# Optimization experiments

Hardware: AMD Instinct MI355X
Metric: run time of the kernel (lower is better)

Reference implementation:

```python
import jax, jax.numpy as jnp
import numpy as np

N, T = 32, 2048
ENC_DIM, DEC_DIM, ATT_DIM = 1024, 1024, 512
CONV_CH, LOC_CTX = 10, 64  # F conv kernel = 2*64+1 = 129 taps


def setup_inputs() -> dict:
    key = jax.random.key(0)
    ks = jax.random.split(key, 12)
    inv = lambda d: 1.0 / np.sqrt(d)
    return {
        "enc_pad": jax.random.normal(ks[0], (N, T, ENC_DIM), jnp.float32),
        "enc_len": jax.random.randint(ks[1], (N,), T // 2, T + 1),
        "dec_prev": jax.random.normal(ks[2], (N, DEC_DIM), jnp.float32),
        "ali_prev": jax.random.uniform(ks[3], (N, T), jnp.float32),
        # enc_proj: Linear(enc_dim, att_dim)
        "W_enc": jax.random.normal(ks[4], (ENC_DIM, ATT_DIM), jnp.float32) * inv(ENC_DIM),
        "b_enc": jax.random.normal(ks[5], (ATT_DIM,), jnp.float32) * 0.01,
        # dec_proj: Linear(dec_dim, att_dim, bias=False)
        "W_dec": jax.random.normal(ks[6], (DEC_DIM, ATT_DIM), jnp.float32) * inv(DEC_DIM),
        # F: Conv1d(1, conv_channels, 129, padding=64)  -> weight [C_out, C_in=1, K]
        "F_w": jax.random.normal(ks[7], (CONV_CH, 1, 2 * LOC_CTX + 1), jnp.float32) * inv(2 * LOC_CTX + 1),
        "F_b": jax.random.normal(ks[8], (CONV_CH,), jnp.float32) * 0.01,
        # att: Conv1d(conv_channels, att_dim, 1, bias=False) == pointwise mix [A, C]
        "W_att": jax.random.normal(ks[9], (ATT_DIM, CONV_CH), jnp.float32) * inv(CONV_CH),
        # w: Linear(att_dim, 1, bias=False)
        "w_vec": jax.random.normal(ks[10], (ATT_DIM,), jnp.float32) * inv(ATT_DIM),
    }


def reference(enc_pad, enc_len, dec_prev, ali_prev, W_enc, b_enc, W_dec, F_w, F_b, W_att, w_vec):
    n, t, _ = enc_pad.shape
    # enc_part: N x T x A (cached across decode steps in the original)
    enc_part = jnp.einsum("ntd,da->nta", enc_pad, W_enc) + b_enc
    # padding mask: True where t >= enc_len
    pad_mask = jnp.arange(t)[None, :] >= enc_len[:, None]  # N x T
    f_out = jax.lax.conv_general_dilated(
        ali_prev[:, None, :], F_w, window_strides=(1,),
        padding=[(LOC_CTX, LOC_CTX)],
        dimension_numbers=("NCH", "OIH", "NCH")) + F_b[None, :, None]
    # pointwise conv (att) then transpose(1,2): N x T x A
    att_part = jnp.einsum("nct,ac->nta", f_out, W_att)
    dec_part = dec_prev @ W_dec  # N x A
    sum_part = jnp.tanh(att_part + dec_part[:, None, :] + enc_part)  # N x T x A
    score = jnp.einsum("nta,a->nt", sum_part, w_vec)  # N x T
    score = jnp.where(pad_mask, -jnp.inf, score)
    ali = jax.nn.softmax(score, axis=-1)  # N x T
    ctx = jnp.einsum("nt,ntd->nd", ali, enc_pad)  # N x D_enc
    return ali, ctx
```

## Files before the change

### kernel.cpp

```cpp
#include <hip/hip_runtime.h>

typedef __attribute__((ext_vector_type(4))) float f32x4;
typedef __attribute__((ext_vector_type(8))) short s16x8;
typedef __attribute__((ext_vector_type(8))) unsigned short u16x8;
typedef __attribute__((address_space(1))) unsigned int g_uint;
typedef __attribute__((address_space(3))) unsigned int lds_uint;

#define T_LEN 2048
#define ENC_D 1024
#define ATT_D 512
#define CONV_C 10

static __device__ __forceinline__ unsigned short f2bf(float f) {
  unsigned int u = __float_as_uint(f);
  u += 0x7FFFu + ((u >> 16) & 1u);
  return (unsigned short)(u >> 16);
}

static __device__ __forceinline__ void gload16(const void* g, void* l) {
  __builtin_amdgcn_global_load_lds((const g_uint*)g, (lds_uint*)l, 16, 0, 0);
}

__global__ void k_wt(const float* __restrict__ W, unsigned short* __restrict__ Wt2) {
  __shared__ float tile[64][65];
  int k0 = blockIdx.x * 64, a0 = blockIdx.y * 64;
  int tid = threadIdx.x;
  int r = tid >> 2, cg = tid & 3;
  #pragma unroll
  for (int i = 0; i < 4; ++i) {
    f32x4 v = *reinterpret_cast<const f32x4*>(&W[(size_t)(k0 + r) * ATT_D + a0 + cg * 16 + i * 4]);
    tile[r][cg * 16 + i * 4 + 0] = v[0];
    tile[r][cg * 16 + i * 4 + 1] = v[1];
    tile[r][cg * 16 + i * 4 + 2] = v[2];
    tile[r][cg * 16 + i * 4 + 3] = v[3];
  }
  __syncthreads();
  int r2 = tid >> 2, kg = tid & 3;
  u16x8 o0, o1;
  #pragma unroll
  for (int j = 0; j < 8; ++j) o0[j] = f2bf(tile[kg * 16 + j][r2]);
  #pragma unroll
  for (int j = 0; j < 8; ++j) o1[j] = f2bf(tile[kg * 16 + 8 + j][r2]);
  int a = a0 + r2;
  int kt = blockIdx.x;
  int q0 = kg * 2, q1 = q0 + 1;
  size_t tb = (size_t)kt * 32768 + (a >> 3) * 512;
  int s7 = a & 7;
  *reinterpret_cast<u16x8*>(&Wt2[tb + q0 * 64 + (s7 ^ q0) * 8]) = o0;
  *reinterpret_cast<u16x8*>(&Wt2[tb + q1 * 64 + (s7 ^ q1) * 8]) = o1;
}

__global__ void k_watt(const float* __restrict__ Wa, unsigned short* __restrict__ Wt2) {
  int a = blockIdx.x * 256 + threadIdx.x;
  size_t tb = (size_t)16 * 32768 + (a >> 3) * 512;
  int s7 = a & 7;
  #pragma unroll
  for (int j = 0; j < 8; ++j) {
    u16x8 v;
    #pragma unroll
    for (int e = 0; e < 8; ++e) {
      int c = j * 8 + e;
      v[e] = (c < CONV_C) ? f2bf(Wa[a * CONV_C + c]) : (unsigned short)0;
    }
    *reinterpret_cast<u16x8*>(&Wt2[tb + j * 64 + (s7 ^ j) * 8]) = v;
  }
}

__global__ void k_conv(const float* __restrict__ ali, const float* __restrict__ Fw,
                       const float* __restrict__ Fb, float* __restrict__ fout) {
  int b = blockIdx.x;
  int tb = b & 7, nc = b >> 3;
  int c = nc % CONV_C, n = nc / CONV_C;
  __shared__ float sa[384];
  __shared__ float sw[129];
  int tid = threadIdx.x;
  int t0 = tb * 256;
  for (int i = tid; i < 384; i += 256) {
    int t = t0 - 64 + i;
    sa[i] = (t >= 0 && t < T_LEN) ? ali[n * T_LEN + t] : 0.f;
  }
  if (tid < 129) sw[tid] = Fw[c * 129 + tid];
  __syncthreads();
  float acc = Fb[c];
  #pragma unroll 8
  for (int k = 0; k < 129; ++k) acc += sw[k] * sa[tid + k];
  fout[(size_t)(n * CONV_C + c) * T_LEN + t0 + tid] = acc;
}

__global__ void k_dec(const float* __restrict__ dec_prev, const float* __restrict__ Wd,
                      const float* __restrict__ benc, float* __restrict__ dec_ws) {
  __shared__ float red[256];
  int b = blockIdx.x;
  int n = b >> 4, ac = b & 15;
  int tid = threadIdx.x;
  int dg = tid >> 5, al = tid & 31;
  int a = ac * 32 + al;
  const float* dp = dec_prev + (size_t)n * 1024 + dg * 128;
  const float* wp = Wd + (size_t)(dg * 128) * ATT_D + a;
  float s = 0.f;
  #pragma unroll 4
  for (int i = 0; i < 128; ++i) s += dp[i] * wp[(size_t)i * ATT_D];
  red[tid] = s;
  __syncthreads();
  if (dg == 0) {
    float t = benc[a];
    #pragma unroll
    for (int g = 0; g < 8; ++g) t += red[g * 32 + al];
    dec_ws[(size_t)n * ATT_D + a] = t;
  }
}

__global__ __launch_bounds__(512, 2) void k_score(
    const float* __restrict__ enc, const unsigned short* __restrict__ Wt2,
    const float* __restrict__ fout, const float* __restrict__ dec_ws,
    const float* __restrict__ w_vec, const int* __restrict__ enc_len,
    float* __restrict__ score_ws) {
  __shared__ __align__(16) char smem[163840];

  int bid = blockIdx.x;
  int half = bid >> 8, p = bid & 255;
  int n = p >> 3, i0 = p & 7;
  int tt = half ? (15 - i0) : i0;
  int t0b = tt * 128;
  if (t0b >= enc_len[n]) return;

  int tid = threadIdx.x;
  int w = tid >> 6, lane = tid & 63;
  int l15 = lane & 15, q = lane >> 4;
  int wm = w >> 2, wn = w & 3;

  const float* Ab = enc + ((size_t)n * T_LEN + t0b) * ENC_D;
  int arow = tid >> 2, aq4 = tid & 3;
  const float* Asrc = Ab + (size_t)arow * ENC_D + aq4 * 16;
  int c0 = aq4 * 2, c1 = c0 + 1;
  int awoff0 = 65536 + (arow >> 3) * 1024 + c0 * 128 + ((arow & 7) ^ c0) * 16;
  int awoff1 = 65536 + (arow >> 3) * 1024 + c1 * 128 + ((arow & 7) ^ c1) * 16;

  int x0 = (l15 & 7) ^ q;
  int ck0 = q * 128 + x0 * 16;
  int ck1 = 512 + q * 128 + (x0 ^ 4) * 16;
  int rgA = wm * 8 + (l15 >> 3);
  int rgB = wn * 16 + (l15 >> 3);

  char* b0 = smem;
  char* b1 = smem + 81920;

  f32x4 acc[4][8];
  #pragma unroll
  for (int m = 0; m < 4; ++m)
    #pragma unroll
    for (int nf = 0; nf < 8; ++nf)
      acc[m][nf] = (f32x4){0.f, 0.f, 0.f, 0.f};

  f32x4 xA0, xA1, xA2, xA3;

  auto STAGE = [&](int kt, char* buf) {
    const float* pA = Asrc + (size_t)kt * 64;
    xA0 = *reinterpret_cast<const f32x4*>(pA);
    xA1 = *reinterpret_cast<const f32x4*>(pA + 4);
    xA2 = *reinterpret_cast<const f32x4*>(pA + 8);
    xA3 = *reinterpret_cast<const f32x4*>(pA + 12);
    const unsigned short* s = Wt2 + (size_t)kt * 32768 + tid * 8;
    #pragma unroll
    for (int i = 0; i < 8; ++i)
      gload16(s + i * 4096, buf + tid * 16 + i * 8192);
  };
  auto WRITEA = [&](char* buf) {
    union { u16x8 v; unsigned int u[4]; } p0, p1;
    asm("v_cvt_pk_bf16_f32 %0, %1, %2" : "=v"(p0.u[0]) : "v"(xA0[0]), "v"(xA0[1]));
    asm("v_cvt_pk_bf16_f32 %0, %1, %2" : "=v"(p0.u[1]) : "v"(xA0[2]), "v"(xA0[3]));
    asm("v_cvt_pk_bf16_f32 %0, %1, %2" : "=v"(p0.u[2]) : "v"(xA1[0]), "v"(xA1[1]));
    asm("v_cvt_pk_bf16_f32 %0, %1, %2" : "=v"(p0.u[3]) : "v"(xA1[2]), "v"(xA1[3]));
    asm("v_cvt_pk_bf16_f32 %0, %1, %2" : "=v"(p1.u[0]) : "v"(xA2[0]), "v"(xA2[1]));
    asm("v_cvt_pk_bf16_f32 %0, %1, %2" : "=v"(p1.u[1]) : "v"(xA2[2]), "v"(xA2[3]));
    asm("v_cvt_pk_bf16_f32 %0, %1, %2" : "=v"(p1.u[2]) : "v"(xA3[0]), "v"(xA3[1]));
    asm("v_cvt_pk_bf16_f32 %0, %1, %2" : "=v"(p1.u[3]) : "v"(xA3[2]), "v"(xA3[3]));
    *reinterpret_cast<u16x8*>(buf + awoff0) = p0.v;
    *reinterpret_cast<u16x8*>(buf + awoff1) = p1.v;
  };
  auto compute = [&](const char* buf) {
    s16x8 af0[4], af1[4];
    #pragma unroll
    for (int m = 0; m < 4; ++m) {
      af0[m] = *reinterpret_cast<const s16x8*>(buf + 65536 + (rgA + m * 2) * 1024 + ck0);
      af1[m] = *reinterpret_cast<const s16x8*>(buf + 65536 + (rgA + m * 2) * 1024 + ck1);
    }
    __builtin_amdgcn_s_setprio(1);
    #pragma unroll
    for (int nf = 0; nf < 8; ++nf) {
      s16x8 bf0 = *reinterpret_cast<const s16x8*>(buf + (rgB + nf * 2) * 1024 + ck0);
      s16x8 bf1 = *reinterpret_cast<const s16x8*>(buf + (rgB + nf * 2) * 1024 + ck1);
      #pragma unroll
      for (int m = 0; m < 4; ++m) {
        acc[m][nf] = __builtin_amdgcn_mfma_f32_16x16x32_bf16(af0[m], bf0, acc[m][nf], 0, 0, 0);
        acc[m][nf] = __builtin_amdgcn_mfma_f32_16x16x32_bf16(af1[m], bf1, acc[m][nf], 0, 0, 0);
      }
    }
    __builtin_amdgcn_s_setprio(0);
  };

  if (tid < 128) {
    float fv[CONV_C];
    #pragma unroll
    for (int c = 0; c < CONV_C; ++c)
      fv[c] = fout[((size_t)n * CONV_C + c) * T_LEN + t0b + tid];
    char* base = b0 + 65536 + (tid >> 3) * 1024;
    int s7 = tid & 7;
    #pragma unroll
    for (int j = 0; j < 8; ++j) {
      u16x8 v;
      #pragma unroll
      for (int e = 0; e < 8; ++e) {
        int c = j * 8 + e;
        v[e] = (c < CONV_C) ? f2bf(fv[c]) : (unsigned short)0;
      }
      *reinterpret_cast<u16x8*>(base + j * 128 + (s7 ^ j) * 16) = v;
    }
  }
  {
    const unsigned short* s = Wt2 + (size_t)16 * 32768 + tid * 8;
    #pragma unroll
    for (int i = 0; i < 8; ++i)
      gload16(s + i * 4096, b0 + tid * 16 + i * 8192);
  }
  STAGE(0, b1);
  asm volatile("s_waitcnt vmcnt(0) lgkmcnt(0)" ::: "memory");
  __builtin_amdgcn_sched_barrier(0);
  __builtin_amdgcn_s_barrier();
  compute(b0);
  WRITEA(b1);

  char* pc = b1; char* pn = b0;
  for (int k = 0; k < 16; ++k) {
    asm volatile("s_waitcnt vmcnt(0) lgkmcnt(0)" ::: "memory");
    __builtin_amdgcn_sched_barrier(0);
    __builtin_amdgcn_s_barrier();
    if (k + 1 < 16) STAGE(k + 1, pn);
    compute(pc);
    if (k + 1 < 16) WRITEA(pn);
    char* t = pc; pc = pn; pn = t;
  }
  __syncthreads();

  float* d_lds = (float*)smem;
  float* w_lds = (float*)(smem + 2048);
  float* red   = (float*)(smem + 4096);
  d_lds[tid] = dec_ws[(size_t)n * ATT_D + tid];
  w_lds[tid] = w_vec[tid];
  __syncthreads();

  #pragma unroll
  for (int m = 0; m < 4; ++m) {
    #pragma unroll
    for (int j = 0; j < 4; ++j) {
      int ttl = wm * 64 + m * 16 + q * 4 + j;
      float s = 0.f;
      #pragma unroll
      for (int nf = 0; nf < 8; ++nf) {
        int cl = wn * 128 + nf * 16 + l15;
        float x = acc[m][nf][j] + d_lds[cl];
        float e = __expf(2.f * x);
        float th = 1.f - 2.f / (e + 1.f);
        s += w_lds[cl] * th;
      }
      float v = s;
      v += __shfl_xor(v, 1);
      v += __shfl_xor(v, 2);
      v += __shfl_xor(v, 4);
      v += __shfl_xor(v, 8);
      if (l15 == 0) red[wn * 128 + ttl] = v;
    }
  }
  __syncthreads();
  if (tid < 128) {
    float s = red[tid] + red[128 + tid] + red[256 + tid] + red[384 + tid];
    score_ws[(size_t)n * T_LEN + t0b + tid] = s;
  }
}

__global__ void k_softmax(const float* __restrict__ score_ws, const int* __restrict__ enc_len,
                          float* __restrict__ ali_out) {
  __shared__ float wmx[4], wsum[4];
  int n = blockIdx.x, tid = threadIdx.x;
  int len = enc_len[n];
  int w = tid >> 6, lane = tid & 63;
  float s[8], e[8];
  float mx = -1e30f;
  #pragma unroll
  for (int i = 0; i < 8; ++i) {
    int t = i * 256 + tid;
    float v = score_ws[n * T_LEN + t];
    s[i] = v;
    if (t < len) mx = fmaxf(mx, v);
  }
  #pragma unroll
  for (int off = 32; off; off >>= 1) mx = fmaxf(mx, __shfl_xor(mx, off));
  if (lane == 0) wmx[w] = mx;
  __syncthreads();
  mx = fmaxf(fmaxf(wmx[0], wmx[1]), fmaxf(wmx[2], wmx[3]));
  float sum = 0.f;
  #pragma unroll
  for (int i = 0; i < 8; ++i) {
    int t = i * 256 + tid;
    float v = (t < len) ? __expf(s[i] - mx) : 0.f;
    e[i] = v;
    sum += v;
  }
  #pragma unroll
  for (int off = 32; off; off >>= 1) sum += __shfl_xor(sum, off);
  if (lane == 0) wsum[w] = sum;
  __syncthreads();
  sum = wsum[0] + wsum[1] + wsum[2] + wsum[3];
  float inv = 1.f / sum;
  #pragma unroll
  for (int i = 0; i < 8; ++i) ali_out[n * T_LEN + i * 256 + tid] = e[i] * inv;
}

__global__ void k_ctx(const float* __restrict__ ali, const float* __restrict__ enc,
                      const int* __restrict__ enc_len, float* __restrict__ part) {
  int b = blockIdx.x;
  int n = b >> 5, tc = b & 31;
  int tid = threadIdx.x;
  if (tc * 64 >= enc_len[n]) {
    *reinterpret_cast<f32x4*>(&part[(size_t)b * ENC_D + tid * 4]) = (f32x4){0.f, 0.f, 0.f, 0.f};
    return;
  }
  f32x4 acc = (f32x4){0.f, 0.f, 0.f, 0.f};
  const float* ep = enc + (size_t)(n * T_LEN + tc * 64) * ENC_D + tid * 4;
  const float* ap = ali + n * T_LEN + tc * 64;
  #pragma unroll 4
  for (int i = 0; i < 64; ++i) {
    float a = ap[i];
    f32x4 ev = *reinterpret_cast<const f32x4*>(ep + (size_t)i * ENC_D);
    acc += ev * a;
  }
  *reinterpret_cast<f32x4*>(&part[(size_t)b * ENC_D + tid * 4]) = acc;
}

__global__ void k_ctx_red(const float* __restrict__ part, float* __restrict__ ctx_out) {
  int g = blockIdx.x * 256 + threadIdx.x;
  int n = g >> 10, d = g & 1023;
  float s = 0.f;
  #pragma unroll 8
  for (int tc = 0; tc < 32; ++tc) s += part[(size_t)(n * 32 + tc) * ENC_D + d];
  ctx_out[g] = s;
}

extern "C" void kernel_launch(void* const* d_in, const int* in_sizes, int n_in,
                              void* d_out, int out_size, void* d_ws, size_t ws_size,
                              hipStream_t stream) {
  const float* enc      = (const float*)d_in[0];
  const int*   enc_len  = (const int*)d_in[1];
  const float* dec_prev = (const float*)d_in[2];
  const float* ali_prev = (const float*)d_in[3];
  const float* W_enc    = (const float*)d_in[4];
  const float* b_enc    = (const float*)d_in[5];
  const float* W_dec    = (const float*)d_in[6];
  const float* F_w      = (const float*)d_in[7];
  const float* F_b      = (const float*)d_in[8];
  const float* W_att    = (const float*)d_in[9];
  const float* w_vec    = (const float*)d_in[10];
  float* out = (float*)d_out;

  char* ws = (char*)d_ws;
  unsigned short* Wt2 = (unsigned short*)ws;
  float* fout   = (float*)(ws + 1114112);
  float* dec_ws = (float*)(ws + 3735552);
  float* score  = (float*)(ws + 3801088);
  float* part   = (float*)(ws + 4063232);

  hipLaunchKernelGGL(k_wt, dim3(16, 8), dim3(256), 0, stream, W_enc, Wt2);
  hipLaunchKernelGGL(k_watt, dim3(2), dim3(256), 0, stream, W_att, Wt2);
  hipLaunchKernelGGL(k_conv, dim3(2560), dim3(256), 0, stream, ali_prev, F_w, F_b, fout);
  hipLaunchKernelGGL(k_dec, dim3(512), dim3(256), 0, stream, dec_prev, W_dec, b_enc, dec_ws);
  hipLaunchKernelGGL(k_score, dim3(512), dim3(512), 0, stream, enc, Wt2, fout, dec_ws, w_vec, enc_len, score);
  hipLaunchKernelGGL(k_softmax, dim3(32), dim3(256), 0, stream, score, enc_len, out);
  hipLaunchKernelGGL(k_ctx, dim3(1024), dim3(256), 0, stream, out, enc, enc_len, part);
  hipLaunchKernelGGL(k_ctx_red, dim3(128), dim3(256), 0, stream, part, out + 65536);
}
```

Measured before the change: 162.4 us.

## Shrink score GEMM tile to 64 rows and K-step 32 with 1024 blocks

The score kernel's block tile drops from 128 time rows with 8 waves to 64 rows with 4 waves, and its K step from 64 to 32. The launch grows to 1024 blocks and the LDS footprint shrinks, so more blocks fit per CU and the grid fills the GPU more evenly. The weight pre-pack layout changes to match the 32-wide K tiles. In exchange, W_enc is re-read twice as often per row of output, and the number of pipeline barriers doubles.

New measurement: 190.5 us. +17.3%, slower.

```diff
diff --git a/kernel.cpp b/kernel.cpp
--- a/kernel.cpp
+++ b/kernel.cpp
@@ -42,27 +42,28 @@
   #pragma unroll
   for (int j = 0; j < 8; ++j) o1[j] = f2bf(tile[kg * 16 + 8 + j][r2]);
   int a = a0 + r2;
-  int kt = blockIdx.x;
-  int q0 = kg * 2, q1 = q0 + 1;
-  size_t tb = (size_t)kt * 32768 + (a >> 3) * 512;
+  int k = k0 + kg * 16;
+  int kt = k >> 5;
+  int q0 = (k >> 3) & 3;
+  size_t tb = (size_t)kt * 16384 + (a >> 3) * 256;
   int s7 = a & 7;
   *reinterpret_cast<u16x8*>(&Wt2[tb + q0 * 64 + (s7 ^ q0) * 8]) = o0;
-  *reinterpret_cast<u16x8*>(&Wt2[tb + q1 * 64 + (s7 ^ q1) * 8]) = o1;
+  *reinterpret_cast<u16x8*>(&Wt2[tb + (q0 + 1) * 64 + (s7 ^ (q0 + 1)) * 8]) = o1;
 }
 
 __global__ void k_watt(const float* __restrict__ Wa, unsigned short* __restrict__ Wt2) {
   int a = blockIdx.x * 256 + threadIdx.x;
-  size_t tb = (size_t)16 * 32768 + (a >> 3) * 512;
+  size_t tb = (size_t)32 * 16384 + (a >> 3) * 256;
   int s7 = a & 7;
   #pragma unroll
-  for (int j = 0; j < 8; ++j) {
+  for (int q2 = 0; q2 < 4; ++q2) {
     u16x8 v;
     #pragma unroll
-    for (int e = 0; e < 8; ++e) {
-      int c = j * 8 + e;
-      v[e] = (c < CONV_C) ? f2bf(Wa[a * CONV_C + c]) : (unsigned short)0;
+    for (int j = 0; j < 8; ++j) {
+      int c = q2 * 8 + j;
+      v[j] = (c < CONV_C) ? f2bf(Wa[a * CONV_C + c]) : (unsigned short)0;
     }
-    *reinterpret_cast<u16x8*>(&Wt2[tb + j * 64 + (s7 ^ j) * 8]) = v;
+    *reinterpret_cast<u16x8*>(&Wt2[tb + q2 * 64 + (s7 ^ q2) * 8]) = v;
   }
 }
 
@@ -110,40 +111,35 @@
   }
 }
 
-__global__ __launch_bounds__(512, 2) void k_score(
+__global__ __launch_bounds__(256, 2) void k_score(
     const float* __restrict__ enc, const unsigned short* __restrict__ Wt2,
     const float* __restrict__ fout, const float* __restrict__ dec_ws,
     const float* __restrict__ w_vec, const int* __restrict__ enc_len,
     float* __restrict__ score_ws) {
-  __shared__ __align__(16) char smem[163840];
+  __shared__ __align__(16) char smem[73728];
 
   int bid = blockIdx.x;
-  int half = bid >> 8, p = bid & 255;
-  int n = p >> 3, i0 = p & 7;
-  int tt = half ? (15 - i0) : i0;
-  int t0b = tt * 128;
+  int n, tt;
+  if (bid < 512) { n = bid >> 4; tt = bid & 15; }
+  else { int p = bid - 512; n = p >> 4; tt = 16 + (p & 15); }
+  int t0b = tt * 64;
   if (t0b >= enc_len[n]) return;
 
   int tid = threadIdx.x;
-  int w = tid >> 6, lane = tid & 63;
+  int wn = tid >> 6, lane = tid & 63;
   int l15 = lane & 15, q = lane >> 4;
-  int wm = w >> 2, wn = w & 3;
 
   const float* Ab = enc + ((size_t)n * T_LEN + t0b) * ENC_D;
-  int arow = tid >> 2, aq4 = tid & 3;
-  const float* Asrc = Ab + (size_t)arow * ENC_D + aq4 * 16;
-  int c0 = aq4 * 2, c1 = c0 + 1;
-  int awoff0 = 65536 + (arow >> 3) * 1024 + c0 * 128 + ((arow & 7) ^ c0) * 16;
-  int awoff1 = 65536 + (arow >> 3) * 1024 + c1 * 128 + ((arow & 7) ^ c1) * 16;
-
-  int x0 = (l15 & 7) ^ q;
-  int ck0 = q * 128 + x0 * 16;
-  int ck1 = 512 + q * 128 + (x0 ^ 4) * 16;
-  int rgA = wm * 8 + (l15 >> 3);
-  int rgB = wn * 16 + (l15 >> 3);
+  int arow = tid >> 2, aq = tid & 3;
+  const float* Asrc = Ab + (size_t)arow * ENC_D + aq * 8;
+
+  int awoff = 32768 + (arow >> 3) * 512 + aq * 128 + ((arow & 7) ^ aq) * 16;
+  int swl = (l15 & 7) ^ q;
+  int aql = 32768 + (l15 >> 3) * 512 + q * 128 + swl * 16;
+  int bql = (wn * 16 + (l15 >> 3)) * 512 + q * 128 + swl * 16;
 
   char* b0 = smem;
-  char* b1 = smem + 81920;
+  char* b1 = smem + 36864;
 
   f32x4 acc[4][8];
   #pragma unroll
@@ -152,76 +148,64 @@
     for (int nf = 0; nf < 8; ++nf)
       acc[m][nf] = (f32x4){0.f, 0.f, 0.f, 0.f};
 
-  f32x4 xA0, xA1, xA2, xA3;
+  f32x4 xA0, xA1;
 
   auto STAGE = [&](int kt, char* buf) {
-    const float* pA = Asrc + (size_t)kt * 64;
+    const float* pA = Asrc + (size_t)kt * 32;
     xA0 = *reinterpret_cast<const f32x4*>(pA);
     xA1 = *reinterpret_cast<const f32x4*>(pA + 4);
-    xA2 = *reinterpret_cast<const f32x4*>(pA + 8);
-    xA3 = *reinterpret_cast<const f32x4*>(pA + 12);
-    const unsigned short* s = Wt2 + (size_t)kt * 32768 + tid * 8;
+    const unsigned short* s = Wt2 + (size_t)kt * 16384 + tid * 8;
     #pragma unroll
     for (int i = 0; i < 8; ++i)
-      gload16(s + i * 4096, buf + tid * 16 + i * 8192);
+      gload16(s + i * 2048, buf + tid * 16 + i * 4096);
   };
   auto WRITEA = [&](char* buf) {
-    union { u16x8 v; unsigned int u[4]; } p0, p1;
-    asm("v_cvt_pk_bf16_f32 %0, %1, %2" : "=v"(p0.u[0]) : "v"(xA0[0]), "v"(xA0[1]));
-    asm("v_cvt_pk_bf16_f32 %0, %1, %2" : "=v"(p0.u[1]) : "v"(xA0[2]), "v"(xA0[3]));
-    asm("v_cvt_pk_bf16_f32 %0, %1, %2" : "=v"(p0.u[2]) : "v"(xA1[0]), "v"(xA1[1]));
-    asm("v_cvt_pk_bf16_f32 %0, %1, %2" : "=v"(p0.u[3]) : "v"(xA1[2]), "v"(xA1[3]));
-    asm("v_cvt_pk_bf16_f32 %0, %1, %2" : "=v"(p1.u[0]) : "v"(xA2[0]), "v"(xA2[1]));
-    asm("v_cvt_pk_bf16_f32 %0, %1, %2" : "=v"(p1.u[1]) : "v"(xA2[2]), "v"(xA2[3]));
-    asm("v_cvt_pk_bf16_f32 %0, %1, %2" : "=v"(p1.u[2]) : "v"(xA3[0]), "v"(xA3[1]));
-    asm("v_cvt_pk_bf16_f32 %0, %1, %2" : "=v"(p1.u[3]) : "v"(xA3[2]), "v"(xA3[3]));
-    *reinterpret_cast<u16x8*>(buf + awoff0) = p0.v;
-    *reinterpret_cast<u16x8*>(buf + awoff1) = p1.v;
+    union { u16x8 v; unsigned int u[4]; } pk;
+    asm("v_cvt_pk_bf16_f32 %0, %1, %2" : "=v"(pk.u[0]) : "v"(xA0[0]), "v"(xA0[1]));
+    asm("v_cvt_pk_bf16_f32 %0, %1, %2" : "=v"(pk.u[1]) : "v"(xA0[2]), "v"(xA0[3]));
+    asm("v_cvt_pk_bf16_f32 %0, %1, %2" : "=v"(pk.u[2]) : "v"(xA1[0]), "v"(xA1[1]));
+    asm("v_cvt_pk_bf16_f32 %0, %1, %2" : "=v"(pk.u[3]) : "v"(xA1[2]), "v"(xA1[3]));
+    *reinterpret_cast<u16x8*>(buf + awoff) = pk.v;
   };
   auto compute = [&](const char* buf) {
-    s16x8 af0[4], af1[4];
-    #pragma unroll
-    for (int m = 0; m < 4; ++m) {
-      af0[m] = *reinterpret_cast<const s16x8*>(buf + 65536 + (rgA + m * 2) * 1024 + ck0);
-      af1[m] = *reinterpret_cast<const s16x8*>(buf + 65536 + (rgA + m * 2) * 1024 + ck1);
-    }
+    s16x8 af[4];
+    #pragma unroll
+    for (int m = 0; m < 4; ++m)
+      af[m] = *reinterpret_cast<const s16x8*>(buf + aql + m * 1024);
     __builtin_amdgcn_s_setprio(1);
     #pragma unroll
     for (int nf = 0; nf < 8; ++nf) {
-      s16x8 bf0 = *reinterpret_cast<const s16x8*>(buf + (rgB + nf * 2) * 1024 + ck0);
-      s16x8 bf1 = *reinterpret_cast<const s16x8*>(buf + (rgB + nf * 2) * 1024 + ck1);
+      s16x8 bf = *reinterpret_cast<const s16x8*>(buf + bql + nf * 1024);
       #pragma unroll
-      for (int m = 0; m < 4; ++m) {
-        acc[m][nf] = __builtin_amdgcn_mfma_f32_16x16x32_bf16(af0[m], bf0, acc[m][nf], 0, 0, 0);
-        acc[m][nf] = __builtin_amdgcn_mfma_f32_16x16x32_bf16(af1[m], bf1, acc[m][nf], 0, 0, 0);
-      }
+      for (int m = 0; m < 4; ++m)
+        acc[m][nf] = __builtin_amdgcn_mfma_f32_16x16x32_bf16(af[m], bf, acc[m][nf], 0, 0, 0);
     }
     __builtin_amdgcn_s_setprio(0);
   };
 
-  if (tid < 128) {
+  if (tid < 64) {
     float fv[CONV_C];
     #pragma unroll
     for (int c = 0; c < CONV_C; ++c)
       fv[c] = fout[((size_t)n * CONV_C + c) * T_LEN + t0b + tid];
-    char* base = b0 + 65536 + (tid >> 3) * 1024;
+    char* base = b0 + 32768 + (tid >> 3) * 512;
     int s7 = tid & 7;
     #pragma unroll
-    for (int j = 0; j < 8; ++j) {
+    for (int q2 = 0; q2 < 4; ++q2) {
       u16x8 v;
       #pragma unroll
       for (int e = 0; e < 8; ++e) {
-        int c = j * 8 + e;
+        int c = q2 * 8 + e;
         v[e] = (c < CONV_C) ? f2bf(fv[c]) : (unsigned short)0;
       }
-      *reinterpret_cast<u16x8*>(base + j * 128 + (s7 ^ j) * 16) = v;
+      *reinterpret_cast<u16x8*>(base + q2 * 128 + (s7 ^ q2) * 16) = v;
     }
   }
   {
-    const unsigned short* s = Wt2 + (size_t)16 * 32768 + tid * 8;
+    const unsigned short* s = Wt2 + (size_t)32 * 16384 + tid * 8;
     #pragma unroll
     for (int i = 0; i < 8; ++i)
-      gload16(s + i * 4096, b0 + tid * 16 + i * 8192);
+      gload16(s + i * 2048, b0 + tid * 16 + i * 4096);
   }
   STAGE(0, b1);
   asm volatile("s_waitcnt vmcnt(0) lgkmcnt(0)" ::: "memory");
@@ -230,15 +214,14 @@
   compute(b0);
   WRITEA(b1);
 
-  char* pc = b1; char* pn = b0;
-  for (int k = 0; k < 16; ++k) {
+  char* B2[2] = {b1, b0};
+  for (int k = 0; k < 32; ++k) {
     asm volatile("s_waitcnt vmcnt(0) lgkmcnt(0)" ::: "memory");
     __builtin_amdgcn_sched_barrier(0);
     __builtin_amdgcn_s_barrier();
-    if (k + 1 < 16) STAGE(k + 1, pn);
-    compute(pc);
-    if (k + 1 < 16) WRITEA(pn);
-    char* t = pc; pc = pn; pn = t;
+    if (k + 1 < 32) STAGE(k + 1, B2[(k + 1) & 1]);
+    compute(B2[k & 1]);
+    if (k + 1 < 32) WRITEA(B2[(k + 1) & 1]);
   }
   __syncthreads();
 
@@ -246,14 +229,16 @@
   float* w_lds = (float*)(smem + 2048);
   float* red   = (float*)(smem + 4096);
   d_lds[tid] = dec_ws[(size_t)n * ATT_D + tid];
+  d_lds[tid + 256] = dec_ws[(size_t)n * ATT_D + tid + 256];
   w_lds[tid] = w_vec[tid];
+  w_lds[tid + 256] = w_vec[tid + 256];
   __syncthreads();
 
   #pragma unroll
   for (int m = 0; m < 4; ++m) {
     #pragma unroll
     for (int j = 0; j < 4; ++j) {
-      int ttl = wm * 64 + m * 16 + q * 4 + j;
+      int row = m * 16 + q * 4 + j;
       float s = 0.f;
       #pragma unroll
       for (int nf = 0; nf < 8; ++nf) {
@@ -268,12 +253,12 @@
       v += __shfl_xor(v, 2);
       v += __shfl_xor(v, 4);
       v += __shfl_xor(v, 8);
-      if (l15 == 0) red[wn * 128 + ttl] = v;
+      if (l15 == 0) red[wn * 64 + row] = v;
     }
   }
   __syncthreads();
-  if (tid < 128) {
-    float s = red[tid] + red[128 + tid] + red[256 + tid] + red[384 + tid];
+  if (tid < 64) {
+    float s = red[tid] + red[64 + tid] + red[128 + tid] + red[192 + tid];
     score_ws[(size_t)n * T_LEN + t0b + tid] = s;
   }
 }
@@ -364,16 +349,16 @@
 
   char* ws = (char*)d_ws;
   unsigned short* Wt2 = (unsigned short*)ws;
-  float* fout   = (float*)(ws + 1114112);
-  float* dec_ws = (float*)(ws + 3735552);
-  float* score  = (float*)(ws + 3801088);
-  float* part   = (float*)(ws + 4063232);
+  float* fout   = (float*)(ws + 1081344);
+  float* dec_ws = (float*)(ws + 3702784);
+  float* score  = (float*)(ws + 3768320);
+  float* part   = (float*)(ws + 4030464);
 
   hipLaunchKernelGGL(k_wt, dim3(16, 8), dim3(256), 0, stream, W_enc, Wt2);
   hipLaunchKernelGGL(k_watt, dim3(2), dim3(256), 0, stream, W_att, Wt2);
   hipLaunchKernelGGL(k_conv, dim3(2560), dim3(256), 0, stream, ali_prev, F_w, F_b, fout);
   hipLaunchKernelGGL(k_dec, dim3(512), dim3(256), 0, stream, dec_prev, W_dec, b_enc, dec_ws);
-  hipLaunchKernelGGL(k_score, dim3(512), dim3(512), 0, stream, enc, Wt2, fout, dec_ws, w_vec, enc_len, score);
+  hipLaunchKernelGGL(k_score, dim3(1024), dim3(256), 0, stream, enc, Wt2, fout, dec_ws, w_vec, enc_len, score);
   hipLaunchKernelGGL(k_softmax, dim3(32), dim3(256), 0, stream, score, enc_len, out);
   hipLaunchKernelGGL(k_ctx, dim3(1024), dim3(256), 0, stream, out, enc, enc_len, part);
   hipLaunchKernelGGL(k_ctx_red, dim3(128), dim3(256), 0, stream, part, out + 65536);
```
